# Kernel optimization log

Hardware: AMD Instinct MI355X
Metric: run time of the kernel (lower is better)

The kernel has to match this reference:

```python
import jax, jax.numpy as jnp
import numpy as np

# Dims derived from Config for the 'ffn' pool
L, S, SE, D, K, B = 7, 200, 240, 32, 3, 512


def setup_inputs() -> dict:
    key = jax.random.key(0)
    k1, k2, k3, k4 = jax.random.split(key, 4)
    x = jax.random.normal(k1, (L, B, D), dtype=jnp.float32)
    vec_clusters = jax.random.normal(k2, (L, S, D), dtype=jnp.float32) * 0.02
    vec = jax.random.normal(k3, (L, S, SE, D), dtype=jnp.float32) * 0.02
    gain_factors = jnp.ones((L, S, SE, 2), dtype=jnp.float32)
    block_indices = jax.random.randint(k4, (L, S, SE, 2), 0, 600).astype(jnp.int32)
    return {
        'x': x,
        'vec_clusters': vec_clusters,
        'vec': vec,
        'gain_factors': gain_factors,
        'block_indices': block_indices,
    }


def reference(x, vec_clusters, vec, gain_factors, block_indices):
    # Router: score each token's query against cluster centroids. [L,B,S]
    logits = jnp.einsum('lbd,lsd->lbs', x, vec_clusters)
    top_vals, top_idx = jax.lax.top_k(logits, K)            # [L,B,K]
    probs = jax.nn.softmax(top_vals, axis=-1)               # [L,B,K]

    # Per-layer gather of the selected clusters' capacity slots.
    gather = jax.vmap(lambda tbl, idx: tbl[idx])            # map over L
    g_vec = gather(vec, top_idx)                            # [L,B,K,SE,D]
    g_gain = gather(gain_factors[..., 0], top_idx)          # [L,B,K,SE]
    g_blk = gather(block_indices[..., 0], top_idx)          # [L,B,K,SE]

    # Empty capacity slots have block index 0 (randint started at 1 in init).
    w = jax.nn.sigmoid(g_gain) * (g_blk != 0).astype(g_gain.dtype)  # [L,B,K,SE]

    # Compose parameter vectors within each selected cluster, then mix top-k.
    comp = jnp.einsum('lbke,lbked->lbkd', w, g_vec)         # [L,B,K,D]
    out = jnp.einsum('lbk,lbkd->lbd', probs, comp)          # [L,B,D]
    return out
```

## Files before the change

### kernel.cpp

```cpp
#include <hip/hip_runtime.h>
#include <math.h>

namespace {
constexpr int L = 7, S = 200, SE = 240, D = 32, B = 512;
constexpr int NTOK = L * B;
constexpr int NCLUST = L * S;

template <int CTRL>
__device__ __forceinline__ float dppf(float x) {
  return __int_as_float(__builtin_amdgcn_update_dpp(
      0, __float_as_int(x), CTRL, 0xF, 0xF, true));
}
template <int CTRL>
__device__ __forceinline__ int dppi(int x) {
  return __builtin_amdgcn_update_dpp(0, x, CTRL, 0xF, 0xF, true);
}
__device__ __forceinline__ float swz16f(float x) {
  return __int_as_float(__builtin_amdgcn_ds_swizzle(__float_as_int(x), 0x401F));
}
__device__ __forceinline__ int swz16i(int x) {
  return __builtin_amdgcn_ds_swizzle(x, 0x401F);
}

__global__ __launch_bounds__(64) void compose_kernel(
    const float* __restrict__ vec,
    const float* __restrict__ gain,
    const int* __restrict__ blk,
    float* __restrict__ C)
{
  const int ls = blockIdx.x;
  const int lane = threadIdx.x;
  __shared__ float sw[SE];
  for (int e = lane; e < SE; e += 64) {
    const float2 g2 = reinterpret_cast<const float2*>(gain)[ls * SE + e];
    const int2 b2 = reinterpret_cast<const int2*>(blk)[ls * SE + e];
    sw[e] = (b2.x != 0) ? 1.0f / (1.0f + __expf(-g2.x)) : 0.0f;
  }
  __syncthreads();
  const int d4 = lane & 7;
  const int eg = lane >> 3;
  const float4* v4 = reinterpret_cast<const float4*>(vec) + (size_t)ls * SE * 8;
  float4 acc = make_float4(0.f, 0.f, 0.f, 0.f);
#pragma unroll 10
  for (int k = 0; k < 30; ++k) {
    const int e = eg + 8 * k;
    const float we = sw[e];
    const float4 v = v4[e * 8 + d4];
    acc.x += we * v.x; acc.y += we * v.y; acc.z += we * v.z; acc.w += we * v.w;
  }
  acc.x += dppf<0x128>(acc.x); acc.y += dppf<0x128>(acc.y);
  acc.z += dppf<0x128>(acc.z); acc.w += dppf<0x128>(acc.w);
  acc.x += swz16f(acc.x); acc.y += swz16f(acc.y);
  acc.z += swz16f(acc.z); acc.w += swz16f(acc.w);
  acc.x += __shfl_xor(acc.x, 32); acc.y += __shfl_xor(acc.y, 32);
  acc.z += __shfl_xor(acc.z, 32); acc.w += __shfl_xor(acc.w, 32);
  if (eg == 0) reinterpret_cast<float4*>(C + ls * D)[d4] = acc;
}

__global__ __launch_bounds__(256) void route_kernel(
    const float* __restrict__ x,
    const float* __restrict__ vc,
    const float* __restrict__ C,
    float* __restrict__ out)
{
  const int wave = threadIdx.x >> 6;
  const int lane = threadIdx.x & 63;
  const int tok = blockIdx.x * 4 + wave;
  const int l = tok >> 9;
  const int q = lane & 7;
  const int r8 = lane >> 3;

  const float4 xq = reinterpret_cast<const float4*>(x + tok * D)[q];
  const float* vcl = vc + l * S * D;

  float v0 = -INFINITY, v1 = -INFINITY, v2 = -INFINITY;
  int i0 = 0x7fffffff, i1 = 0x7fffffff, i2 = 0x7fffffff;
  for (int s0 = 0; s0 < S; s0 += 8) {
    const int row = s0 + r8;
    const float4 v = reinterpret_cast<const float4*>(vcl + row * D)[q];
    float part = v.x * xq.x + v.y * xq.y + v.z * xq.z + v.w * xq.w;
    part += dppf<0xB1>(part);
    part += dppf<0x4E>(part);
    part += dppf<0x141>(part);
    if (part > v0) { v2 = v1; i2 = i1; v1 = v0; i1 = i0; v0 = part; i0 = row; }
    else if (part > v1) { v2 = v1; i2 = i1; v1 = part; i1 = row; }
    else if (part > v2) { v2 = part; i2 = row; }
  }

#pragma unroll
  for (int step = 0; step < 3; ++step) {
    float u0, u1, u2; int j0, j1, j2;
    if (step == 0) {
      u0 = dppf<0x128>(v0); u1 = dppf<0x128>(v1); u2 = dppf<0x128>(v2);
      j0 = dppi<0x128>(i0); j1 = dppi<0x128>(i1); j2 = dppi<0x128>(i2);
    } else if (step == 1) {
      u0 = swz16f(v0); u1 = swz16f(v1); u2 = swz16f(v2);
      j0 = swz16i(i0); j1 = swz16i(i1); j2 = swz16i(i2);
    } else {
      u0 = __shfl_xor(v0, 32); u1 = __shfl_xor(v1, 32); u2 = __shfl_xor(v2, 32);
      j0 = __shfl_xor(i0, 32); j1 = __shfl_xor(i1, 32); j2 = __shfl_xor(i2, 32);
    }
#pragma unroll
    for (int t = 0; t < 3; ++t) {
      const float u = (t == 0) ? u0 : (t == 1) ? u1 : u2;
      const int j = (t == 0) ? j0 : (t == 1) ? j1 : j2;
      const bool b0 = (u > v0) || (u == v0 && j < i0);
      const bool b1 = (u > v1) || (u == v1 && j < i1);
      const bool b2 = (u > v2) || (u == v2 && j < i2);
      if (b0) { v2 = v1; i2 = i1; v1 = v0; i1 = i0; v0 = u; i0 = j; }
      else if (b1) { v2 = v1; i2 = i1; v1 = u; i1 = j; }
      else if (b2) { v2 = u; i2 = j; }
    }
  }

  const float e1 = __expf(v1 - v0);
  const float e2 = __expf(v2 - v0);
  const float inv = 1.f / (1.f + e1 + e2);

  if (lane < D) {
    const float* Cl = C + l * S * D;
    out[tok * D + lane] = inv * Cl[i0 * D + lane] +
                          e1 * inv * Cl[i1 * D + lane] +
                          e2 * inv * Cl[i2 * D + lane];
  }
}

}

extern "C" void kernel_launch(void* const* d_in, const int* in_sizes, int n_in,
                              void* d_out, int out_size, void* d_ws, size_t ws_size,
                              hipStream_t stream) {
  const float* x = (const float*)d_in[0];
  const float* vc = (const float*)d_in[1];
  const float* vec = (const float*)d_in[2];
  const float* gain = (const float*)d_in[3];
  const int* blk = (const int*)d_in[4];
  float* out = (float*)d_out;
  float* C = (float*)d_ws;

  compose_kernel<<<NCLUST, 64, 0, stream>>>(vec, gain, blk, C);
  route_kernel<<<NTOK / 4, 256, 0, stream>>>(x, vc, C, out);
}
```

Measured before the change: 27.61 us.

## Run compose and routing concurrently in one launch, then gather in a second kernel

Merges the cluster-compose work and the router top-k work into a single launch with disjoint block ranges, so the two independent phases overlap instead of running back to back. The router saves top-3 indices and softmax weights to workspace, and a new small gather kernel mixes the composed vectors afterward. Compose blocks now handle four clusters per 256-thread block. The cost is an extra workspace round trip for indices and probabilities, plus a third stage of gather work, while the kernel count stays at two.

```diff
diff --git a/kernel.cpp b/kernel.cpp
--- a/kernel.cpp
+++ b/kernel.cpp
@@ -5,6 +5,9 @@
 constexpr int L = 7, S = 200, SE = 240, D = 32, B = 512;
 constexpr int NTOK = L * B;
 constexpr int NCLUST = L * S;
+constexpr int NCOMP_BLK = NCLUST / 4;
+constexpr int NROUTE_BLK = NTOK / 4;
+constexpr int GRID1 = NCOMP_BLK + NROUTE_BLK;
 
 template <int CTRL>
 __device__ __forceinline__ float dppf(float x) {
@@ -22,107 +25,117 @@
   return __builtin_amdgcn_ds_swizzle(x, 0x401F);
 }
 
-__global__ __launch_bounds__(64) void compose_kernel(
+__global__ __launch_bounds__(256) void fused1_kernel(
+    const float* __restrict__ x,
+    const float* __restrict__ vc,
     const float* __restrict__ vec,
     const float* __restrict__ gain,
     const int* __restrict__ blk,
-    float* __restrict__ C)
-{
-  const int ls = blockIdx.x;
-  const int lane = threadIdx.x;
-  __shared__ float sw[SE];
-  for (int e = lane; e < SE; e += 64) {
-    const float2 g2 = reinterpret_cast<const float2*>(gain)[ls * SE + e];
-    const int2 b2 = reinterpret_cast<const int2*>(blk)[ls * SE + e];
-    sw[e] = (b2.x != 0) ? 1.0f / (1.0f + __expf(-g2.x)) : 0.0f;
-  }
-  __syncthreads();
-  const int d4 = lane & 7;
-  const int eg = lane >> 3;
-  const float4* v4 = reinterpret_cast<const float4*>(vec) + (size_t)ls * SE * 8;
-  float4 acc = make_float4(0.f, 0.f, 0.f, 0.f);
-#pragma unroll 10
-  for (int k = 0; k < 30; ++k) {
-    const int e = eg + 8 * k;
-    const float we = sw[e];
-    const float4 v = v4[e * 8 + d4];
-    acc.x += we * v.x; acc.y += we * v.y; acc.z += we * v.z; acc.w += we * v.w;
-  }
-  acc.x += dppf<0x128>(acc.x); acc.y += dppf<0x128>(acc.y);
-  acc.z += dppf<0x128>(acc.z); acc.w += dppf<0x128>(acc.w);
-  acc.x += swz16f(acc.x); acc.y += swz16f(acc.y);
-  acc.z += swz16f(acc.z); acc.w += swz16f(acc.w);
-  acc.x += __shfl_xor(acc.x, 32); acc.y += __shfl_xor(acc.y, 32);
-  acc.z += __shfl_xor(acc.z, 32); acc.w += __shfl_xor(acc.w, 32);
-  if (eg == 0) reinterpret_cast<float4*>(C + ls * D)[d4] = acc;
-}
-
-__global__ __launch_bounds__(256) void route_kernel(
-    const float* __restrict__ x,
-    const float* __restrict__ vc,
-    const float* __restrict__ C,
-    float* __restrict__ out)
+    float* __restrict__ C,
+    int4* __restrict__ tki,
+    float4* __restrict__ tkp)
 {
   const int wave = threadIdx.x >> 6;
   const int lane = threadIdx.x & 63;
-  const int tok = blockIdx.x * 4 + wave;
-  const int l = tok >> 9;
-  const int q = lane & 7;
-  const int r8 = lane >> 3;
 
-  const float4 xq = reinterpret_cast<const float4*>(x + tok * D)[q];
-  const float* vcl = vc + l * S * D;
+  if (blockIdx.x < NCOMP_BLK) {
+    __shared__ float wl[4][SE];
+    const int ls = blockIdx.x * 4 + wave;
+    for (int e = lane; e < SE; e += 64) {
+      const float2 g2 = reinterpret_cast<const float2*>(gain)[ls * SE + e];
+      const int2 b2 = reinterpret_cast<const int2*>(blk)[ls * SE + e];
+      wl[wave][e] = (b2.x != 0) ? 1.0f / (1.0f + __expf(-g2.x)) : 0.0f;
+    }
+    __syncthreads();
+    const int d4 = lane & 7;
+    const int eg = lane >> 3;
+    const float4* v4 = reinterpret_cast<const float4*>(vec) + (size_t)ls * SE * 8;
+    float4 acc = make_float4(0.f, 0.f, 0.f, 0.f);
+#pragma unroll 10
+    for (int k = 0; k < 30; ++k) {
+      const int e = eg + 8 * k;
+      const float we = wl[wave][e];
+      const float4 v = v4[e * 8 + d4];
+      acc.x += we * v.x; acc.y += we * v.y; acc.z += we * v.z; acc.w += we * v.w;
+    }
+    acc.x += dppf<0x128>(acc.x); acc.y += dppf<0x128>(acc.y);
+    acc.z += dppf<0x128>(acc.z); acc.w += dppf<0x128>(acc.w);
+    acc.x += swz16f(acc.x); acc.y += swz16f(acc.y);
+    acc.z += swz16f(acc.z); acc.w += swz16f(acc.w);
+    acc.x += __shfl_xor(acc.x, 32); acc.y += __shfl_xor(acc.y, 32);
+    acc.z += __shfl_xor(acc.z, 32); acc.w += __shfl_xor(acc.w, 32);
+    if (eg == 0) reinterpret_cast<float4*>(C + ls * D)[d4] = acc;
+  } else {
+    const int tok = (blockIdx.x - NCOMP_BLK) * 4 + wave;
+    const int l = tok >> 9;
+    const int q = lane & 7;
+    const int r8 = lane >> 3;
 
-  float v0 = -INFINITY, v1 = -INFINITY, v2 = -INFINITY;
-  int i0 = 0x7fffffff, i1 = 0x7fffffff, i2 = 0x7fffffff;
-  for (int s0 = 0; s0 < S; s0 += 8) {
-    const int row = s0 + r8;
-    const float4 v = reinterpret_cast<const float4*>(vcl + row * D)[q];
-    float part = v.x * xq.x + v.y * xq.y + v.z * xq.z + v.w * xq.w;
-    part += dppf<0xB1>(part);
-    part += dppf<0x4E>(part);
-    part += dppf<0x141>(part);
-    if (part > v0) { v2 = v1; i2 = i1; v1 = v0; i1 = i0; v0 = part; i0 = row; }
-    else if (part > v1) { v2 = v1; i2 = i1; v1 = part; i1 = row; }
-    else if (part > v2) { v2 = part; i2 = row; }
-  }
+    const float4 xq = reinterpret_cast<const float4*>(x + tok * D)[q];
+    const float* vcl = vc + l * S * D;
 
-#pragma unroll
-  for (int step = 0; step < 3; ++step) {
-    float u0, u1, u2; int j0, j1, j2;
-    if (step == 0) {
-      u0 = dppf<0x128>(v0); u1 = dppf<0x128>(v1); u2 = dppf<0x128>(v2);
-      j0 = dppi<0x128>(i0); j1 = dppi<0x128>(i1); j2 = dppi<0x128>(i2);
-    } else if (step == 1) {
-      u0 = swz16f(v0); u1 = swz16f(v1); u2 = swz16f(v2);
-      j0 = swz16i(i0); j1 = swz16i(i1); j2 = swz16i(i2);
-    } else {
-      u0 = __shfl_xor(v0, 32); u1 = __shfl_xor(v1, 32); u2 = __shfl_xor(v2, 32);
-      j0 = __shfl_xor(i0, 32); j1 = __shfl_xor(i1, 32); j2 = __shfl_xor(i2, 32);
+    float v0 = -INFINITY, v1 = -INFINITY, v2 = -INFINITY;
+    int i0 = 0x7fffffff, i1 = 0x7fffffff, i2 = 0x7fffffff;
+    for (int s0 = 0; s0 < S; s0 += 8) {
+      const int row = s0 + r8;
+      const float4 v = reinterpret_cast<const float4*>(vcl + row * D)[q];
+      float part = v.x * xq.x + v.y * xq.y + v.z * xq.z + v.w * xq.w;
+      part += dppf<0xB1>(part);
+      part += dppf<0x4E>(part);
+      part += dppf<0x141>(part);
+      if (part > v0) { v2 = v1; i2 = i1; v1 = v0; i1 = i0; v0 = part; i0 = row; }
+      else if (part > v1) { v2 = v1; i2 = i1; v1 = part; i1 = row; }
+      else if (part > v2) { v2 = part; i2 = row; }
     }
 #pragma unroll
-    for (int t = 0; t < 3; ++t) {
-      const float u = (t == 0) ? u0 : (t == 1) ? u1 : u2;
-      const int j = (t == 0) ? j0 : (t == 1) ? j1 : j2;
-      const bool b0 = (u > v0) || (u == v0 && j < i0);
-      const bool b1 = (u > v1) || (u == v1 && j < i1);
-      const bool b2 = (u > v2) || (u == v2 && j < i2);
-      if (b0) { v2 = v1; i2 = i1; v1 = v0; i1 = i0; v0 = u; i0 = j; }
-      else if (b1) { v2 = v1; i2 = i1; v1 = u; i1 = j; }
-      else if (b2) { v2 = u; i2 = j; }
+    for (int step = 0; step < 3; ++step) {
+      float u0, u1, u2; int j0, j1, j2;
+      if (step == 0) {
+        u0 = dppf<0x128>(v0); u1 = dppf<0x128>(v1); u2 = dppf<0x128>(v2);
+        j0 = dppi<0x128>(i0); j1 = dppi<0x128>(i1); j2 = dppi<0x128>(i2);
+      } else if (step == 1) {
+        u0 = swz16f(v0); u1 = swz16f(v1); u2 = swz16f(v2);
+        j0 = swz16i(i0); j1 = swz16i(i1); j2 = swz16i(i2);
+      } else {
+        u0 = __shfl_xor(v0, 32); u1 = __shfl_xor(v1, 32); u2 = __shfl_xor(v2, 32);
+        j0 = __shfl_xor(i0, 32); j1 = __shfl_xor(i1, 32); j2 = __shfl_xor(i2, 32);
+      }
+#pragma unroll
+      for (int t = 0; t < 3; ++t) {
+        const float u = (t == 0) ? u0 : (t == 1) ? u1 : u2;
+        const int j = (t == 0) ? j0 : (t == 1) ? j1 : j2;
+        const bool b0 = (u > v0) || (u == v0 && j < i0);
+        const bool b1 = (u > v1) || (u == v1 && j < i1);
+        const bool b2 = (u > v2) || (u == v2 && j < i2);
+        if (b0) { v2 = v1; i2 = i1; v1 = v0; i1 = i0; v0 = u; i0 = j; }
+        else if (b1) { v2 = v1; i2 = i1; v1 = u; i1 = j; }
+        else if (b2) { v2 = u; i2 = j; }
+      }
+    }
+    if (lane == 0) {
+      const float e1 = __expf(v1 - v0);
+      const float e2 = __expf(v2 - v0);
+      const float inv = 1.f / (1.f + e1 + e2);
+      tki[tok] = make_int4(i0, i1, i2, 0);
+      tkp[tok] = make_float4(inv, e1 * inv, e2 * inv, 0.f);
     }
   }
+}
 
-  const float e1 = __expf(v1 - v0);
-  const float e2 = __expf(v2 - v0);
-  const float inv = 1.f / (1.f + e1 + e2);
-
-  if (lane < D) {
-    const float* Cl = C + l * S * D;
-    out[tok * D + lane] = inv * Cl[i0 * D + lane] +
-                          e1 * inv * Cl[i1 * D + lane] +
-                          e2 * inv * Cl[i2 * D + lane];
-  }
+__global__ __launch_bounds__(256) void gather_kernel(
+    const float* __restrict__ C,
+    const int4* __restrict__ tki,
+    const float4* __restrict__ tkp,
+    float* __restrict__ out)
+{
+  const int gid = blockIdx.x * 256 + threadIdx.x;
+  const int tok = gid >> 5;
+  const int d = gid & 31;
+  const int l = tok >> 9;
+  const int4 id = tki[tok];
+  const float4 p = tkp[tok];
+  const float* Cl = C + l * S * D;
+  out[gid] = p.x * Cl[id.x * D + d] + p.y * Cl[id.y * D + d] + p.z * Cl[id.z * D + d];
 }
 
 }
@@ -136,8 +149,12 @@
   const float* gain = (const float*)d_in[3];
   const int* blk = (const int*)d_in[4];
   float* out = (float*)d_out;
-  float* C = (float*)d_ws;
 
-  compose_kernel<<<NCLUST, 64, 0, stream>>>(vec, gain, blk, C);
-  route_kernel<<<NTOK / 4, 256, 0, stream>>>(x, vc, C, out);
+  char* ws = (char*)d_ws;
+  float* C = (float*)ws;
+  int4* tki = (int4*)(ws + 179200);
+  float4* tkp = (float4*)(ws + 179200 + 57344);
+
+  fused1_kernel<<<GRID1, 256, 0, stream>>>(x, vc, vec, gain, blk, C, tki, tkp);
+  gather_kernel<<<NTOK * D / 256, 256, 0, stream>>>(C, tki, tkp, out);
 }
```

Measured after the change: 23.46 us. 15.0% less time.

## Fuse cluster composition into routing kernel, composing only selected clusters per token

Applied to the files above, without the earlier changes.

Replaces the two-kernel pipeline, which precomposed all L*S clusters into a workspace and then gathered them, with one kernel. Each wave computes its token's top-3 and then recomputes the weighted composition of only those three clusters directly from vec, gain and block_indices. It also remaps block indices so each XCD handles a contiguous token range, which should improve cache locality within a layer. This removes one launch and the full precompose pass over vec, but composition work becomes redundant per token (about 3 clusters × 30KB each) and serialized behind the top-k. It therefore relies heavily on L2/MALL hits.

```diff
diff --git a/kernel.cpp b/kernel.cpp
--- a/kernel.cpp
+++ b/kernel.cpp
@@ -4,7 +4,7 @@
 namespace {
 constexpr int L = 7, S = 200, SE = 240, D = 32, B = 512;
 constexpr int NTOK = L * B;
-constexpr int NCLUST = L * S;
+constexpr int NBLK = NTOK / 4;
 
 template <int CTRL>
 __device__ __forceinline__ float dppf(float x) {
@@ -22,53 +22,23 @@
   return __builtin_amdgcn_ds_swizzle(x, 0x401F);
 }
 
-__global__ __launch_bounds__(64) void compose_kernel(
+__global__ __launch_bounds__(256) void fused_kernel(
+    const float* __restrict__ x,
+    const float* __restrict__ vc,
     const float* __restrict__ vec,
     const float* __restrict__ gain,
     const int* __restrict__ blk,
-    float* __restrict__ C)
-{
-  const int ls = blockIdx.x;
-  const int lane = threadIdx.x;
-  __shared__ float sw[SE];
-  for (int e = lane; e < SE; e += 64) {
-    const float2 g2 = reinterpret_cast<const float2*>(gain)[ls * SE + e];
-    const int2 b2 = reinterpret_cast<const int2*>(blk)[ls * SE + e];
-    sw[e] = (b2.x != 0) ? 1.0f / (1.0f + __expf(-g2.x)) : 0.0f;
-  }
-  __syncthreads();
-  const int d4 = lane & 7;
-  const int eg = lane >> 3;
-  const float4* v4 = reinterpret_cast<const float4*>(vec) + (size_t)ls * SE * 8;
-  float4 acc = make_float4(0.f, 0.f, 0.f, 0.f);
-#pragma unroll 10
-  for (int k = 0; k < 30; ++k) {
-    const int e = eg + 8 * k;
-    const float we = sw[e];
-    const float4 v = v4[e * 8 + d4];
-    acc.x += we * v.x; acc.y += we * v.y; acc.z += we * v.z; acc.w += we * v.w;
-  }
-  acc.x += dppf<0x128>(acc.x); acc.y += dppf<0x128>(acc.y);
-  acc.z += dppf<0x128>(acc.z); acc.w += dppf<0x128>(acc.w);
-  acc.x += swz16f(acc.x); acc.y += swz16f(acc.y);
-  acc.z += swz16f(acc.z); acc.w += swz16f(acc.w);
-  acc.x += __shfl_xor(acc.x, 32); acc.y += __shfl_xor(acc.y, 32);
-  acc.z += __shfl_xor(acc.z, 32); acc.w += __shfl_xor(acc.w, 32);
-  if (eg == 0) reinterpret_cast<float4*>(C + ls * D)[d4] = acc;
-}
-
-__global__ __launch_bounds__(256) void route_kernel(
-    const float* __restrict__ x,
-    const float* __restrict__ vc,
-    const float* __restrict__ C,
     float* __restrict__ out)
 {
   const int wave = threadIdx.x >> 6;
   const int lane = threadIdx.x & 63;
-  const int tok = blockIdx.x * 4 + wave;
+  const int slot = (blockIdx.x & 7) * (NBLK / 8) + (blockIdx.x >> 3);
+  const int tok = slot * 4 + wave;
   const int l = tok >> 9;
   const int q = lane & 7;
   const int r8 = lane >> 3;
+
+  __shared__ float w[4][SE];
 
   const float4 xq = reinterpret_cast<const float4*>(x + tok * D)[q];
   const float* vcl = vc + l * S * D;
@@ -86,7 +56,6 @@
     else if (part > v1) { v2 = v1; i2 = i1; v1 = part; i1 = row; }
     else if (part > v2) { v2 = part; i2 = row; }
   }
-
 #pragma unroll
   for (int step = 0; step < 3; ++step) {
     float u0, u1, u2; int j0, j1, j2;
@@ -112,17 +81,42 @@
       else if (b2) { v2 = u; i2 = j; }
     }
   }
-
   const float e1 = __expf(v1 - v0);
   const float e2 = __expf(v2 - v0);
-  const float inv = 1.f / (1.f + e1 + e2);
+  const float sinv = 1.f / (1.f + e1 + e2);
+  const float p0 = sinv, p1 = e1 * sinv, p2 = e2 * sinv;
 
-  if (lane < D) {
-    const float* Cl = C + l * S * D;
-    out[tok * D + lane] = inv * Cl[i0 * D + lane] +
-                          e1 * inv * Cl[i1 * D + lane] +
-                          e2 * inv * Cl[i2 * D + lane];
+  float4 oacc = make_float4(0.f, 0.f, 0.f, 0.f);
+#pragma unroll
+  for (int k = 0; k < 3; ++k) {
+    const int sk = (k == 0) ? i0 : (k == 1) ? i1 : i2;
+    const float pk = (k == 0) ? p0 : (k == 1) ? p1 : p2;
+    const int ls = l * S + sk;
+    for (int e = lane; e < SE; e += 64) {
+      const float2 g2 = reinterpret_cast<const float2*>(gain)[ls * SE + e];
+      const int2 b2 = reinterpret_cast<const int2*>(blk)[ls * SE + e];
+      w[wave][e] = (b2.x != 0) ? 1.0f / (1.0f + __expf(-g2.x)) : 0.0f;
+    }
+    const float4* v4 = reinterpret_cast<const float4*>(vec) + (size_t)ls * SE * 8;
+    float4 acc = make_float4(0.f, 0.f, 0.f, 0.f);
+#pragma unroll 10
+    for (int kk = 0; kk < 30; ++kk) {
+      const int e = kk * 8 + r8;
+      const float we = w[wave][e];
+      const float4 v = v4[e * 8 + q];
+      acc.x += we * v.x; acc.y += we * v.y; acc.z += we * v.z; acc.w += we * v.w;
+    }
+    acc.x += dppf<0x128>(acc.x); acc.y += dppf<0x128>(acc.y);
+    acc.z += dppf<0x128>(acc.z); acc.w += dppf<0x128>(acc.w);
+    acc.x += swz16f(acc.x); acc.y += swz16f(acc.y);
+    acc.z += swz16f(acc.z); acc.w += swz16f(acc.w);
+    acc.x += __shfl_xor(acc.x, 32); acc.y += __shfl_xor(acc.y, 32);
+    acc.z += __shfl_xor(acc.z, 32); acc.w += __shfl_xor(acc.w, 32);
+    oacc.x += pk * acc.x; oacc.y += pk * acc.y;
+    oacc.z += pk * acc.z; oacc.w += pk * acc.w;
   }
+  if (lane < 8)
+    reinterpret_cast<float4*>(out + tok * D)[lane] = oacc;
 }
 
 }
@@ -136,8 +130,6 @@
   const float* gain = (const float*)d_in[3];
   const int* blk = (const int*)d_in[4];
   float* out = (float*)d_out;
-  float* C = (float*)d_ws;
 
-  compose_kernel<<<NCLUST, 64, 0, stream>>>(vec, gain, blk, C);
-  route_kernel<<<NTOK / 4, 256, 0, stream>>>(x, vc, C, out);
+  fused_kernel<<<NBLK, 256, 0, stream>>>(x, vc, vec, gain, blk, out);
 }
```

Measured after the change: 54.96 us. 1.99x slower.
